# Performance work log

Measured on AMD Instinct MI355X. Metric: run time of the kernel, lower is better.

Reference implementation:

```python
import jax, jax.numpy as jnp
import numpy as np

ROPE_THETA = 10000.0

def _apply_rope(x, theta=ROPE_THETA):
    # x: [B, H, L, d_head]
    L, d_k = x.shape[-2], x.shape[-1]
    inv_freq = 1.0 / (theta ** (jnp.arange(0, d_k, 2, dtype=jnp.float32) / d_k))  # [d_k/2]
    ang = jnp.arange(L, dtype=jnp.float32)[:, None] * inv_freq[None, :]           # [L, d_k/2]
    ang = jnp.repeat(ang, 2, axis=-1)                                             # [L, d_k] interleaved
    xr = x.reshape(x.shape[:-1] + (d_k // 2, 2))
    rot = jnp.stack((-xr[..., 1], xr[..., 0]), axis=-1).reshape(x.shape)
    return x * jnp.cos(ang) + rot * jnp.sin(ang)

def setup_inputs() -> dict:
    key = jax.random.key(0)
    k1, k2, k3 = jax.random.split(key, 3)
    B, L, D = 2, 2048, 2048
    std_qkv = np.sqrt(2.0 / (D + 3 * D)).astype(np.float32)
    std_o = np.sqrt(2.0 / (D + D)).astype(np.float32)
    return {
        "x": jax.random.normal(k1, (B, L, D), dtype=jnp.float32),
        "W_qkv": jax.random.normal(k2, (3 * D, D), dtype=jnp.float32) * std_qkv,
        "W_o": jax.random.normal(k3, (D, D), dtype=jnp.float32) * std_o,
    }

def reference(x, W_qkv, W_o):
    B, L, D = x.shape
    H = 16
    dh = D // H
    qkv = jnp.einsum('bld,ed->ble', x, W_qkv)            # [B, L, 3D]
    q, k, v = jnp.split(qkv, 3, axis=-1)
    # [B, H, L, dh]
    q = q.reshape(B, L, H, dh).transpose(0, 2, 1, 3)
    k = k.reshape(B, L, H, dh).transpose(0, 2, 1, 3)
    v = v.reshape(B, L, H, dh).transpose(0, 2, 1, 3)
    q = _apply_rope(q)
    k = _apply_rope(k)
    scale = 1.0 / np.sqrt(dh).astype(np.float32)
    att = jnp.einsum('bhqd,bhkd->bhqk', q, k) * scale    # [B, H, L, L]
    causal = jnp.tril(jnp.ones((L, L), dtype=bool))
    att = jnp.where(causal, att, -jnp.inf)
    p = jax.nn.softmax(att, axis=-1)
    y = jnp.einsum('bhqk,bhkd->bhqd', p, v)              # [B, H, L, dh]
    y = y.transpose(0, 2, 1, 3).reshape(B, L, D)
    return jnp.einsum('bld,ed->ble', y, W_o)
```

## Files before the change

kernel.cpp:

```cpp
#include <hip/hip_runtime.h>
#include <math.h>

typedef __bf16 bf16x8 __attribute__((ext_vector_type(8)));
typedef float f32x4 __attribute__((ext_vector_type(4)));
typedef unsigned short us8 __attribute__((ext_vector_type(8)));

#define B_ 2
#define L_ 2048
#define D_ 2048
#define H_ 16
#define DH 128

__device__ __forceinline__ unsigned short f2b(float f) {
  union { float f; unsigned u; } v; v.f = f;
  unsigned u = v.u;
  return (unsigned short)((u + 0x7fffu + ((u >> 16) & 1u)) >> 16);
}
__device__ __forceinline__ float b2f(unsigned short h) {
  union { unsigned u; float f; } v; v.u = ((unsigned)h) << 16;
  return v.f;
}

#define GLD16(g, l) __builtin_amdgcn_global_load_lds(                          \
    (const __attribute__((address_space(1))) void*)(g),                        \
    (__attribute__((address_space(3))) void*)(l), 16, 0, 0)

#define SBAR() __builtin_amdgcn_s_barrier()
#define LGK0() asm volatile("s_waitcnt lgkmcnt(0)")
#define SCB0() __builtin_amdgcn_sched_barrier(0)
#define VMC3() asm volatile("s_waitcnt vmcnt(3)" ::: "memory")
#define VMC0() asm volatile("s_waitcnt vmcnt(0)" ::: "memory")

__device__ __forceinline__ unsigned ldsoff(const void* p) {
  return (unsigned)(unsigned long long)(const __attribute__((address_space(3))) char*)p;
}
__device__ __forceinline__ bf16x8 dsr128(unsigned a) {
  bf16x8 r;
  asm volatile("ds_read_b128 %0, %1" : "=v"(r) : "v"(a));
  return r;
}

__global__ void f32_to_bf16_3(const float* __restrict__ a, int na4,
                              const float* __restrict__ b, int nb4,
                              const float* __restrict__ c, int nc4,
                              unsigned short* __restrict__ oa,
                              unsigned short* __restrict__ ob,
                              unsigned short* __restrict__ oc) {
  const int total = na4 + nb4 + nc4;
  int i = blockIdx.x * blockDim.x + threadIdx.x;
  const int stride = gridDim.x * blockDim.x;
  for (; i < total; i += stride) {
    const float* src;
    unsigned short* dst;
    int j = i;
    if (j < na4) { src = a; dst = oa; }
    else if (j < na4 + nb4) { j -= na4; src = b; dst = ob; }
    else { j -= na4 + nb4; src = c; dst = oc; }
    const float4 v = ((const float4*)src)[j];
    ushort4 o;
    o.x = f2b(v.x); o.y = f2b(v.y); o.z = f2b(v.z); o.w = f2b(v.w);
    ((ushort4*)dst)[j] = o;
  }
}

template <bool OUT_BF16>
__global__ __launch_bounds__(512, 4)
void gemmk32(const unsigned short* __restrict__ A,
             const unsigned short* __restrict__ Bm,
             void* __restrict__ Cv, int M, int N, int K) {
  __shared__ __align__(16) unsigned short lA[3][128 * 32];
  __shared__ __align__(16) unsigned short lB[3][256 * 32];
  const int tid = threadIdx.x;
  const int w = tid >> 6, lane = tid & 63;
  const int lo = lane & 15, hi = lane >> 4;
  const int mh = w >> 2;
  const int wn = (w & 3) * 64;
  const int GM = M >> 7;
  const int nwg = gridDim.x;
  const int f = blockIdx.x;
  const int v = (f & 7) * (nwg >> 3) + (f >> 3);
  const int bn = v / GM, bm = v % GM;
  const int NT = K >> 5;

  const int srow = tid >> 2;
  const int gs = (tid & 3) ^ ((srow >> 1) & 3);
  auto stA = [&](int buf, int tile) {
    GLD16(A + (long)(bm * 128 + srow) * K + tile * 32 + gs * 8,
          &lA[buf][(tid & ~63) * 8]);
  };
  auto stB = [&](int buf, int u, int tile) {
    GLD16(Bm + (long)(bn * 256 + u * 128 + srow) * K + tile * 32 + gs * 8,
          &lB[buf][u * 4096 + (tid & ~63) * 8]);
  };

  unsigned aoff[4], boff[4];
#pragma unroll
  for (int mi = 0; mi < 4; ++mi) {
    const int r = mh * 64 + mi * 16 + lo;
    aoff[mi] = ldsoff(&lA[0][0]) + r * 64 + ((hi ^ ((r >> 1) & 3)) * 16);
  }
#pragma unroll
  for (int ni = 0; ni < 4; ++ni) {
    const int rb = wn + ni * 16 + lo;
    boff[ni] = ldsoff(&lB[0][0]) + rb * 64 + ((hi ^ ((rb >> 1) & 3)) * 16);
  }

  f32x4 acc[4][4] = {};

  stA(0, 0); stB(0, 0, 0); stB(0, 1, 0);
  stA(1, 1); stB(1, 0, 1); stB(1, 1, 1);
  VMC3();
  SBAR();

  for (int t = 0; t < NT; ++t) {
    const int bt = t % 3;
    const int b2 = (t + 2) % 3;
    const bool nx = (t + 2 < NT);
    const unsigned ab = (unsigned)(bt * 8192);
    const unsigned bb = (unsigned)(bt * 16384);
    bf16x8 af[4], bfv[4];
#pragma unroll
    for (int mi = 0; mi < 4; ++mi) af[mi] = dsr128(aoff[mi] + ab);
#pragma unroll
    for (int ni = 0; ni < 4; ++ni) bfv[ni] = dsr128(boff[ni] + bb);
    if (nx) { stA(b2, t + 2); stB(b2, 0, t + 2); stB(b2, 1, t + 2); }
    LGK0(); SCB0();
    __builtin_amdgcn_s_setprio(1);
#pragma unroll
    for (int mi = 0; mi < 4; ++mi)
#pragma unroll
      for (int ni = 0; ni < 4; ++ni)
        acc[mi][ni] = __builtin_amdgcn_mfma_f32_16x16x32_bf16(
            af[mi], bfv[ni], acc[mi][ni], 0, 0, 0);
    __builtin_amdgcn_s_setprio(0);
    if (t < NT - 2) VMC3(); else VMC0();
    SBAR();
  }

  const int r0 = bm * 128 + mh * 64;
  const int c0 = bn * 256 + wn;
#pragma unroll
  for (int mi = 0; mi < 4; ++mi) {
#pragma unroll
    for (int r = 0; r < 4; ++r) {
      const long row = r0 + mi * 16 + hi * 4 + r;
#pragma unroll
      for (int ni = 0; ni < 4; ++ni) {
        const int col = c0 + ni * 16 + lo;
        if (OUT_BF16)
          ((unsigned short*)Cv)[row * N + col] = f2b(acc[mi][ni][r]);
        else
          ((float*)Cv)[row * N + col] = acc[mi][ni][r];
      }
    }
  }
}

__global__ void rope_qk(const unsigned short* __restrict__ qkv,
                        unsigned short* __restrict__ Qo,
                        unsigned short* __restrict__ Ko) {
  const int idx = blockIdx.x * 256 + threadIdx.x;
  const int i = idx & 63;
  const int l = (idx >> 6) & (L_ - 1);
  const int h = (idx >> 17) & (H_ - 1);
  const int b = idx >> 21;
  const float invf = exp2f(-(float)i * 0.20762050593045077f);
  const float ang = (float)l * invf;
  float sn, cs;
  sincosf(ang, &sn, &cs);
  const long base = ((long)b * L_ + l) * (3 * D_) + h * DH + 2 * i;
  const unsigned qin = *(const unsigned*)&qkv[base];
  const unsigned kin = *(const unsigned*)&qkv[base + D_];
  const float q0 = b2f((unsigned short)qin), q1 = b2f((unsigned short)(qin >> 16));
  const float k0 = b2f((unsigned short)kin), k1 = b2f((unsigned short)(kin >> 16));
  const float sc = 0.12751743f;
  const float qo0 = (q0 * cs - q1 * sn) * sc, qo1 = (q1 * cs + q0 * sn) * sc;
  const float ko0 = (k0 * cs - k1 * sn), ko1 = (k1 * cs + k0 * sn);
  const long oo = ((long)(b * H_ + h) * L_ + l) * DH + 2 * i;
  *(unsigned*)&Qo[oo] = (unsigned)f2b(qo0) | ((unsigned)f2b(qo1) << 16);
  *(unsigned*)&Ko[oo] = (unsigned)f2b(ko0) | ((unsigned)f2b(ko1) << 16);
}

__global__ __launch_bounds__(256)
void v_fragpack(const unsigned short* __restrict__ qkv,
                unsigned short* __restrict__ Vf) {
  const int lblk = blockIdx.x;
  const int bh = blockIdx.y;
  const int b = bh >> 4, h = bh & 15;
  __shared__ unsigned short tile[64 * 137];
  const int tid = threadIdx.x;
  const int l0 = lblk * 64;
#pragma unroll
  for (int j = 0; j < 4; ++j) {
    const int c = j * 256 + tid;
    const int row = c >> 4, col8 = c & 15;
    const us8 v = *(const us8*)&qkv[((long)b * L_ + l0 + row) * (3 * D_) +
                                    2 * D_ + h * DH + col8 * 8];
    unsigned short* dst = &tile[row * 137 + col8 * 8];
#pragma unroll
    for (int e = 0; e < 8; ++e) dst[e] = v[e];
  }
  __syncthreads();
#pragma unroll
  for (int j = 0; j < 4; ++j) {
    const int c = j * 256 + tid;
    const int k32l = c >> 9, t2 = (c >> 6) & 7, lane = c & 63;
    const int lo = lane & 15, hi = lane >> 4;
    us8 v;
#pragma unroll
    for (int e = 0; e < 8; ++e)
      v[e] = tile[(k32l * 32 + hi * 8 + e) * 137 + t2 * 16 + lo];
    *(us8*)&Vf[(((size_t)bh * 64 + lblk * 2 + k32l) * 8 + t2) * 512 + lane * 8] = v;
  }
}

__global__ __launch_bounds__(256, 2)
void flash_attn3(const unsigned short* __restrict__ Q,
                 const unsigned short* __restrict__ Kg,
                 const unsigned short* __restrict__ Vf,
                 unsigned short* __restrict__ Y) {
  const int p = blockIdx.x;
  const int tA = p, tB = (L_ / 64 - 1) - p;
  const int h = blockIdx.y, b = blockIdx.z;
  const int tid = threadIdx.x;
  const int wave = tid >> 6, lane = tid & 63;
  const int lo = lane & 15, hi = lane >> 4;
  const int swz = (lo & 7) << 4;
  const int qA = tA * 64 + wave * 16;
  const int qB = tB * 64 + wave * 16;
  const long hoff = ((long)(b * H_ + h)) * L_ * DH;
  const unsigned short* Qh = Q + hoff;
  const unsigned short* Kh = Kg + hoff;
  const unsigned short* Vfh = Vf + ((size_t)(b * H_ + h)) * (64 * 8 * 512);

  __shared__ unsigned short lK[2][64 * 128];
  __shared__ unsigned short pl[4][2][16 * 72];
  unsigned short* plA = &pl[wave][0][0];
  unsigned short* plB = &pl[wave][1][0];

  auto stage = [&](int bufi, int kv0s) {
    unsigned short* bk = &lK[bufi][0];
#pragma unroll
    for (int j = 0; j < 4; ++j) {
      const int c = j * 256 + tid;
      const int row = c >> 4;
      const int soff = ((c & 15) ^ (row & 7)) << 3;
      GLD16(Kh + (long)(kv0s + row) * DH + soff, &bk[(c & ~63) * 8]);
    }
  };

  bf16x8 qfA[4], qfB[4];
#pragma unroll
  for (int s = 0; s < 4; ++s) {
    qfA[s] = *(const bf16x8*)&Qh[(long)(qA + lo) * DH + s * 32 + hi * 8];
    qfB[s] = *(const bf16x8*)&Qh[(long)(qB + lo) * DH + s * 32 + hi * 8];
  }

  float mA = -INFINITY, lsA = 0.f, mB = -INFINITY, lsB = 0.f;
  f32x4 yA[8] = {}, yB[8] = {};

  auto softmax = [&](f32x4 (&st)[4], float& m, float& lsum, f32x4 (&yacc)[8],
                     unsigned short* plw, int qw, int kv0) {
    if (kv0 + 63 > qw) {
      const int d0 = qw + lo - kv0 - hi * 4;
#pragma unroll
      for (int t = 0; t < 4; ++t) {
        const int dt = d0 - t * 16;
#pragma unroll
        for (int r = 0; r < 4; ++r)
          if (r > dt) st[t][r] = -INFINITY;
      }
    }
    float tm0 = fmaxf(fmaxf(st[0][0], st[0][1]), fmaxf(st[0][2], st[0][3]));
    float tm1 = fmaxf(fmaxf(st[1][0], st[1][1]), fmaxf(st[1][2], st[1][3]));
    float tm2 = fmaxf(fmaxf(st[2][0], st[2][1]), fmaxf(st[2][2], st[2][3]));
    float tm3 = fmaxf(fmaxf(st[3][0], st[3][1]), fmaxf(st[3][2], st[3][3]));
    float rm = fmaxf(fmaxf(tm0, tm1), fmaxf(tm2, tm3));
    rm = fmaxf(rm, __shfl_xor(rm, 16));
    rm = fmaxf(rm, __shfl_xor(rm, 32));
    if (!__all(rm <= m + 8.f)) {
      const float mn = fmaxf(m, rm);
      const float alpha = exp2f(m - mn);
      m = mn;
      lsum *= alpha;
      float ar[4];
#pragma unroll
      for (int r = 0; r < 4; ++r) ar[r] = __shfl(alpha, hi * 4 + r);
#pragma unroll
      for (int t2 = 0; t2 < 8; ++t2)
#pragma unroll
        for (int r = 0; r < 4; ++r) yacc[t2][r] *= ar[r];
    }
    float rs = 0.f;
#pragma unroll
    for (int t = 0; t < 4; ++t) {
#pragma unroll
      for (int r2 = 0; r2 < 2; ++r2) {
        const float e0 = exp2f(st[t][2 * r2] - m);
        const float e1 = exp2f(st[t][2 * r2 + 1] - m);
        rs += e0 + e1;
        const unsigned short u0 = __builtin_bit_cast(unsigned short, (__bf16)e0);
        const unsigned short u1 = __builtin_bit_cast(unsigned short, (__bf16)e1);
        *(unsigned*)&plw[lo * 72 + t * 16 + hi * 4 + 2 * r2] =
            (unsigned)u0 | ((unsigned)u1 << 16);
      }
    }
    rs += __shfl_xor(rs, 16);
    rs += __shfl_xor(rs, 32);
    lsum += rs;
  };

  const int nIter = tB + 1;
  stage(0, 0);
  __syncthreads();

  for (int it = 0; it < nIter; ++it) {
    const int kv0 = it * 64;
    const bool aAct = (it <= tA);
    if (it + 1 < nIter) stage((it + 1) & 1, kv0 + 64);
    const char* bkc = (const char*)&lK[it & 1][0];
    f32x4 stA[4] = {}, stB[4] = {};
    if (aAct) {
#pragma unroll
      for (int s = 0; s < 4; ++s) {
        const int inner = (lo * 256 + s * 64 + hi * 16) ^ swz;
#pragma unroll
        for (int t = 0; t < 4; ++t) {
          const bf16x8 kf = *(const bf16x8*)(bkc + t * 4096 + inner);
          stA[t] = __builtin_amdgcn_mfma_f32_16x16x32_bf16(kf, qfA[s], stA[t], 0, 0, 0);
          stB[t] = __builtin_amdgcn_mfma_f32_16x16x32_bf16(kf, qfB[s], stB[t], 0, 0, 0);
        }
      }
    } else {
#pragma unroll
      for (int s = 0; s < 4; ++s) {
        const int inner = (lo * 256 + s * 64 + hi * 16) ^ swz;
#pragma unroll
        for (int t = 0; t < 4; ++t) {
          const bf16x8 kf = *(const bf16x8*)(bkc + t * 4096 + inner);
          stB[t] = __builtin_amdgcn_mfma_f32_16x16x32_bf16(kf, qfB[s], stB[t], 0, 0, 0);
        }
      }
    }
    if (aAct) softmax(stA, mA, lsA, yA, plA, qA, kv0);
    softmax(stB, mB, lsB, yB, plB, qB, kv0);
    const unsigned short* vbase = Vfh + (size_t)(it * 16) * 512 + lane * 8;
#pragma unroll
    for (int kt = 0; kt < 2; ++kt) {
      bf16x8 vf[8];
#pragma unroll
      for (int t2 = 0; t2 < 8; ++t2)
        vf[t2] = *(const bf16x8*)(vbase + (size_t)(kt * 8 + t2) * 512);
      const bf16x8 pfB = *(const bf16x8*)&plB[lo * 72 + kt * 32 + hi * 8];
#pragma unroll
      for (int t2 = 0; t2 < 8; ++t2)
        yB[t2] = __builtin_amdgcn_mfma_f32_16x16x32_bf16(pfB, vf[t2], yB[t2], 0, 0, 0);
      if (aAct) {
        const bf16x8 pfA = *(const bf16x8*)&plA[lo * 72 + kt * 32 + hi * 8];
#pragma unroll
        for (int t2 = 0; t2 < 8; ++t2)
          yA[t2] = __builtin_amdgcn_mfma_f32_16x16x32_bf16(pfA, vf[t2], yA[t2], 0, 0, 0);
      }
    }
    __syncthreads();
  }

  auto wout = [&](f32x4 (&yacc)[8], float lsum, int qw) {
    const float inv = 1.f / lsum;
    float ir[4];
#pragma unroll
    for (int r = 0; r < 4; ++r) ir[r] = __shfl(inv, hi * 4 + r);
#pragma unroll
    for (int r = 0; r < 4; ++r) {
      const long row = qw + hi * 4 + r;
      unsigned short* yrow = Y + ((long)b * L_ + row) * D_ + h * DH;
#pragma unroll
      for (int t2 = 0; t2 < 8; ++t2)
        yrow[t2 * 16 + lo] = f2b(yacc[t2][r] * ir[r]);
    }
  };
  wout(yA, lsA, qA);
  wout(yB, lsB, qB);
}

extern "C" void kernel_launch(void* const* d_in, const int* in_sizes, int n_in,
                              void* d_out, int out_size, void* d_ws, size_t ws_size,
                              hipStream_t stream) {
  const float* x = (const float*)d_in[0];
  const float* wqkv = (const float*)d_in[1];
  const float* wo = (const float*)d_in[2];
  float* out = (float*)d_out;

  unsigned short* ws = (unsigned short*)d_ws;
  const size_t N_X = (size_t)B_ * L_ * D_;
  const size_t N_WQKV = (size_t)3 * D_ * D_;
  const size_t N_WO = (size_t)D_ * D_;
  const size_t N_QKV = (size_t)B_ * L_ * 3 * D_;
  const size_t N_HEAD = (size_t)B_ * H_ * L_ * DH;
  unsigned short* xb = ws;
  unsigned short* wqkb = xb + N_X;
  unsigned short* wob = wqkb + N_WQKV;
  unsigned short* qkv = wob + N_WO;
  unsigned short* Qb = qkv + N_QKV;
  unsigned short* Kb = Qb + N_HEAD;
  unsigned short* Vf = Kb + N_HEAD;
  unsigned short* Yb = Vf + N_HEAD;
  const size_t need = (size_t)(Yb + N_HEAD - ws) * sizeof(unsigned short);
  if (ws_size < need) return;

  f32_to_bf16_3<<<2048, 256, 0, stream>>>(
      x, (int)(N_X / 4), wqkv, (int)(N_WQKV / 4), wo, (int)(N_WO / 4),
      xb, wqkb, wob);

  gemmk32<true><<<(B_ * L_ / 128) * (3 * D_ / 256), 512, 0, stream>>>(
      xb, wqkb, qkv, B_ * L_, 3 * D_, D_);

  rope_qk<<<(B_ * H_ * L_ * 64) / 256, 256, 0, stream>>>(qkv, Qb, Kb);
  v_fragpack<<<dim3(L_ / 64, B_ * H_), 256, 0, stream>>>(qkv, Vf);

  flash_attn3<<<dim3(16, H_, B_), 256, 0, stream>>>(Qb, Kb, Vf, Yb);

  gemmk32<false><<<(B_ * L_ / 128) * (D_ / 256), 512, 0, stream>>>(
      Yb, wob, out, B_ * L_, D_, D_);
}
```

Baseline: 286.0 us.

## Add 256x256 ping-pong GEMM for QKV projection and prefetch V fragments early

Introduces a new GEMM kernel with 256x256 output tiles, K=64 double-buffered LDS stages split into halves, XOR-swizzled LDS layout, and interleaved MFMA clusters with setprio and staged vmcnt waits. It replaces the 128x256 K=32 GEMM for the QKV projection, aiming for higher arithmetic intensity and better overlap of global loads with MFMA work. Separately, in attention, all 16 V fragments are loaded before softmax so their global latency hides behind softmax math. This raises register pressure (acc[8][4] plus fragments, vf[16]) and reduces the grid size, which risks occupancy or tail effects.

Result: no change. 286.1 us (+0.0%).

```diff
diff --git a/kernel.cpp b/kernel.cpp
--- a/kernel.cpp
+++ b/kernel.cpp
@@ -27,9 +27,11 @@
 
 #define SBAR() __builtin_amdgcn_s_barrier()
 #define LGK0() asm volatile("s_waitcnt lgkmcnt(0)")
-#define SCB0() __builtin_amdgcn_sched_barrier(0)
+#define VMC8() asm volatile("s_waitcnt vmcnt(8)" ::: "memory")
+#define VMC4() asm volatile("s_waitcnt vmcnt(4)" ::: "memory")
 #define VMC3() asm volatile("s_waitcnt vmcnt(3)" ::: "memory")
 #define VMC0() asm volatile("s_waitcnt vmcnt(0)" ::: "memory")
+#define SCB0() __builtin_amdgcn_sched_barrier(0)
 
 __device__ __forceinline__ unsigned ldsoff(const void* p) {
   return (unsigned)(unsigned long long)(const __attribute__((address_space(3))) char*)p;
@@ -60,6 +62,125 @@
     ushort4 o;
     o.x = f2b(v.x); o.y = f2b(v.y); o.z = f2b(v.z); o.w = f2b(v.w);
     ((ushort4*)dst)[j] = o;
+  }
+}
+
+#define LOAD_A8(BUF, MH)                                                       \
+  _Pragma("unroll") for (int q = 0; q < 4; ++q) {                              \
+    const int rh = (MH) * 64 + q * 16 + lo;                                    \
+    _Pragma("unroll") for (int s = 0; s < 2; ++s)                              \
+        af[q][s] = *(const bf16x8*)&lA[BUF][wm]                                \
+            [rh * 64 + (((s * 4 + hi) ^ (rh & 7)) * 8)];                       \
+  }
+
+#define LOAD_B8(BUF, NH)                                                       \
+  _Pragma("unroll") for (int j = 0; j < 2; ++j) {                              \
+    const int rb = blb + (NH) * 32 + j * 16 + lo;                              \
+    _Pragma("unroll") for (int s = 0; s < 2; ++s)                              \
+        bfr[NH][j][s] = *(const bf16x8*)&lB[BUF][hb]                           \
+            [rb * 64 + (((s * 4 + hi) ^ (rb & 7)) * 8)];                       \
+  }
+
+#define MFMA16P(MH, NH)                                                        \
+  do {                                                                         \
+    __builtin_amdgcn_s_setprio(1);                                             \
+    _Pragma("unroll") for (int q = 0; q < 4; ++q)                              \
+        _Pragma("unroll") for (int j = 0; j < 2; ++j)                          \
+            _Pragma("unroll") for (int s = 0; s < 2; ++s)                      \
+                acc[(MH) * 4 + q][(NH) * 2 + j] =                              \
+                    __builtin_amdgcn_mfma_f32_16x16x32_bf16(                   \
+                        af[q][s], bfr[NH][j][s],                               \
+                        acc[(MH) * 4 + q][(NH) * 2 + j], 0, 0, 0);             \
+    __builtin_amdgcn_s_setprio(0);                                             \
+  } while (0)
+
+template <bool OUT_BF16>
+__global__ __launch_bounds__(512)
+void gemm8x(const unsigned short* __restrict__ A,
+            const unsigned short* __restrict__ Bm,
+            void* __restrict__ Cv, int M, int N, int K) {
+  __shared__ __align__(16) unsigned short lA[2][2][128 * 64];
+  __shared__ __align__(16) unsigned short lB[2][2][128 * 64];
+  const int tid = threadIdx.x;
+  const int w = tid >> 6, lane = tid & 63;
+  const int lo = lane & 15, hi = lane >> 4;
+  const int wm = w >> 2;
+  const int wn4 = w & 3;
+  const int hb = wn4 >> 1;
+  const int blb = (wn4 & 1) * 64;
+  const int GM = M >> 8;
+  const int f = blockIdx.x;
+  const int v = (f & 7) * (gridDim.x >> 3) + (f >> 3);
+  const int bn = v / GM, bm = v % GM;
+  const int NI = K >> 7;
+
+  const int row64 = tid >> 3;
+  const int gs = (tid & 7) ^ (row64 & 7);
+  auto stA = [&](int buf, int h, int tile) {
+#pragma unroll
+    for (int u = 0; u < 2; ++u)
+      GLD16(A + (long)(bm * 256 + h * 128 + u * 64 + row64) * K + tile * 64 + gs * 8,
+            &lA[buf][h][u * 4096 + (tid & ~63) * 8]);
+  };
+  auto stB = [&](int buf, int h, int tile) {
+#pragma unroll
+    for (int u = 0; u < 2; ++u)
+      GLD16(Bm + (long)(bn * 256 + h * 128 + u * 64 + row64) * K + tile * 64 + gs * 8,
+            &lB[buf][h][u * 4096 + (tid & ~63) * 8]);
+  };
+
+  f32x4 acc[8][4] = {};
+  bf16x8 af[4][2], bfr[2][2][2];
+
+  stB(0, 0, 0); stB(0, 1, 0); stA(0, 0, 0); stA(0, 1, 0);
+  stB(1, 0, 1); stB(1, 1, 1); stA(1, 0, 1); stA(1, 1, 1);
+  VMC8();
+  SBAR();
+
+  for (int i = 0; i < NI; ++i) {
+    const int t2n = 2 * i + 2;
+    const bool nx = (i + 1 < NI);
+    LOAD_A8(0, 0) LOAD_B8(0, 0)
+    SBAR(); LGK0(); MFMA16P(0, 0); SBAR();
+    LOAD_B8(0, 1)
+    SBAR(); LGK0(); MFMA16P(0, 1); SBAR();
+    LOAD_A8(0, 1)
+    if (nx) stB(0, 0, t2n);
+    SBAR(); LGK0(); MFMA16P(1, 1); SBAR();
+    if (nx) stB(0, 1, t2n);
+    SBAR(); MFMA16P(1, 0);
+    if (nx) VMC4(); else VMC0();
+    SBAR();
+    LOAD_A8(1, 0) LOAD_B8(1, 0)
+    if (nx) { stA(0, 0, t2n); stA(0, 1, t2n); }
+    SBAR(); LGK0(); MFMA16P(0, 0); SBAR();
+    LOAD_B8(1, 1)
+    SBAR(); LGK0(); MFMA16P(0, 1); SBAR();
+    LOAD_A8(1, 1)
+    if (nx) { stB(1, 0, t2n + 1); stB(1, 1, t2n + 1); }
+    SBAR(); LGK0(); MFMA16P(1, 1); SBAR();
+    if (nx) { stA(1, 0, t2n + 1); stA(1, 1, t2n + 1); }
+    SBAR(); MFMA16P(1, 0);
+    if (nx) VMC8();
+    SBAR();
+  }
+
+  const int r0 = bm * 256 + wm * 128;
+  const int c0 = bn * 256 + wn4 * 64;
+#pragma unroll
+  for (int mi = 0; mi < 8; ++mi) {
+#pragma unroll
+    for (int r = 0; r < 4; ++r) {
+      const long row = r0 + mi * 16 + hi * 4 + r;
+#pragma unroll
+      for (int ni = 0; ni < 4; ++ni) {
+        const int col = c0 + ni * 16 + lo;
+        if (OUT_BF16)
+          ((unsigned short*)Cv)[row * N + col] = f2b(acc[mi][ni][r]);
+        else
+          ((float*)Cv)[row * N + col] = acc[mi][ni][r];
+      }
+    }
   }
 }
 
@@ -342,24 +463,24 @@
         }
       }
     }
+    const unsigned short* vbase = Vfh + (size_t)(it * 16) * 512 + lane * 8;
+    bf16x8 vf[16];
+#pragma unroll
+    for (int t2 = 0; t2 < 16; ++t2)
+      vf[t2] = *(const bf16x8*)(vbase + (size_t)t2 * 512);
     if (aAct) softmax(stA, mA, lsA, yA, plA, qA, kv0);
     softmax(stB, mB, lsB, yB, plB, qB, kv0);
-    const unsigned short* vbase = Vfh + (size_t)(it * 16) * 512 + lane * 8;
 #pragma unroll
     for (int kt = 0; kt < 2; ++kt) {
-      bf16x8 vf[8];
+      const bf16x8 pfB = *(const bf16x8*)&plB[lo * 72 + kt * 32 + hi * 8];
 #pragma unroll
       for (int t2 = 0; t2 < 8; ++t2)
-        vf[t2] = *(const bf16x8*)(vbase + (size_t)(kt * 8 + t2) * 512);
-      const bf16x8 pfB = *(const bf16x8*)&plB[lo * 72 + kt * 32 + hi * 8];
-#pragma unroll
-      for (int t2 = 0; t2 < 8; ++t2)
-        yB[t2] = __builtin_amdgcn_mfma_f32_16x16x32_bf16(pfB, vf[t2], yB[t2], 0, 0, 0);
+        yB[t2] = __builtin_amdgcn_mfma_f32_16x16x32_bf16(pfB, vf[kt * 8 + t2], yB[t2], 0, 0, 0);
       if (aAct) {
         const bf16x8 pfA = *(const bf16x8*)&plA[lo * 72 + kt * 32 + hi * 8];
 #pragma unroll
         for (int t2 = 0; t2 < 8; ++t2)
-          yA[t2] = __builtin_amdgcn_mfma_f32_16x16x32_bf16(pfA, vf[t2], yA[t2], 0, 0, 0);
+          yA[t2] = __builtin_amdgcn_mfma_f32_16x16x32_bf16(pfA, vf[kt * 8 + t2], yA[t2], 0, 0, 0);
       }
     }
     __syncthreads();
@@ -412,7 +533,7 @@
       x, (int)(N_X / 4), wqkv, (int)(N_WQKV / 4), wo, (int)(N_WO / 4),
       xb, wqkb, wob);
 
-  gemmk32<true><<<(B_ * L_ / 128) * (3 * D_ / 256), 512, 0, stream>>>(
+  gemm8x<true><<<(B_ * L_ / 256) * (3 * D_ / 256), 512, 0, stream>>>(
       xb, wqkb, qkv, B_ * L_, 3 * D_, D_);
 
   rope_qk<<<(B_ * H_ * L_ * 64) / 256, 256, 0, stream>>>(qkv, Qb, Kb);
```

## Add 4-wave 64x128-per-wave GEMM for QKV projection and prefetch V earlier

Applied to the files above, without the earlier changes.

Adds a new GEMM kernel that uses 256 threads, with each wave computing a 64x128 output tile (4x8 MFMA fragments) over a triple-buffered LDS pipeline. The QKV projection now uses it instead of the 8-wave kernel. The goal is more register-level reuse of A and B fragments per LDS read, at the cost of higher register pressure and lower occupancy. In flash attention, all 16 V fragments are now loaded before the softmax, so global load latency overlaps the softmax math, which costs more VGPRs.

After: 278.0 us. -2.8%, faster.

```diff
diff --git a/kernel.cpp b/kernel.cpp
--- a/kernel.cpp
+++ b/kernel.cpp
@@ -28,6 +28,7 @@
 #define SBAR() __builtin_amdgcn_s_barrier()
 #define LGK0() asm volatile("s_waitcnt lgkmcnt(0)")
 #define SCB0() __builtin_amdgcn_sched_barrier(0)
+#define VMC6() asm volatile("s_waitcnt vmcnt(6)" ::: "memory")
 #define VMC3() asm volatile("s_waitcnt vmcnt(3)" ::: "memory")
 #define VMC0() asm volatile("s_waitcnt vmcnt(0)" ::: "memory")
 
@@ -60,6 +61,105 @@
     ushort4 o;
     o.x = f2b(v.x); o.y = f2b(v.y); o.z = f2b(v.z); o.w = f2b(v.w);
     ((ushort4*)dst)[j] = o;
+  }
+}
+
+template <bool OUT_BF16>
+__global__ __launch_bounds__(256, 2)
+void gemmw128(const unsigned short* __restrict__ A,
+              const unsigned short* __restrict__ Bm,
+              void* __restrict__ Cv, int M, int N, int K) {
+  __shared__ __align__(16) unsigned short lA[3][128 * 32];
+  __shared__ __align__(16) unsigned short lB[3][256 * 32];
+  const int tid = threadIdx.x;
+  const int w = tid >> 6, lane = tid & 63;
+  const int lo = lane & 15, hi = lane >> 4;
+  const int mh = w >> 1;
+  const int nh = w & 1;
+  const int GM = M >> 7;
+  const int nwg = gridDim.x;
+  const int f = blockIdx.x;
+  const int v = (f & 7) * (nwg >> 3) + (f >> 3);
+  const int bn = v / GM, bm = v % GM;
+  const int NT = K >> 5;
+
+  const int srow = tid >> 2;
+  const int gs = (tid & 3) ^ ((srow >> 1) & 3);
+  auto stA = [&](int buf, int u, int tile) {
+    GLD16(A + (long)(bm * 128 + u * 64 + srow) * K + tile * 32 + gs * 8,
+          &lA[buf][u * 2048 + tid * 8]);
+  };
+  auto stB = [&](int buf, int u, int tile) {
+    GLD16(Bm + (long)(bn * 256 + u * 64 + srow) * K + tile * 32 + gs * 8,
+          &lB[buf][u * 2048 + tid * 8]);
+  };
+
+  unsigned aoff[4], boff[8];
+#pragma unroll
+  for (int mi = 0; mi < 4; ++mi) {
+    const int r = mh * 64 + mi * 16 + lo;
+    aoff[mi] = ldsoff(&lA[0][0]) + r * 64 + ((hi ^ ((r >> 1) & 3)) * 16);
+  }
+#pragma unroll
+  for (int ni = 0; ni < 8; ++ni) {
+    const int rb = nh * 128 + ni * 16 + lo;
+    boff[ni] = ldsoff(&lB[0][0]) + rb * 64 + ((hi ^ ((rb >> 1) & 3)) * 16);
+  }
+
+  f32x4 acc[4][8] = {};
+
+  stA(0, 0, 0); stA(0, 1, 0);
+  stB(0, 0, 0); stB(0, 1, 0); stB(0, 2, 0); stB(0, 3, 0);
+  stA(1, 0, 1); stA(1, 1, 1);
+  stB(1, 0, 1); stB(1, 1, 1); stB(1, 2, 1); stB(1, 3, 1);
+  VMC6();
+  SBAR();
+
+  for (int t = 0; t < NT; ++t) {
+    const int bt = t % 3;
+    const int b2 = (t + 2) % 3;
+    const bool nx = (t + 2 < NT);
+    const unsigned ab = (unsigned)(bt * 8192);
+    const unsigned bb = (unsigned)(bt * 16384);
+    bf16x8 af[4], bfv[8];
+#pragma unroll
+    for (int mi = 0; mi < 4; ++mi) af[mi] = dsr128(aoff[mi] + ab);
+#pragma unroll
+    for (int ni = 0; ni < 8; ++ni) bfv[ni] = dsr128(boff[ni] + bb);
+    if (nx) {
+      stA(b2, 0, t + 2); stA(b2, 1, t + 2);
+      stB(b2, 0, t + 2); stB(b2, 1, t + 2);
+      stB(b2, 2, t + 2); stB(b2, 3, t + 2);
+    }
+    LGK0(); SCB0();
+    __builtin_amdgcn_s_setprio(1);
+#pragma unroll
+    for (int ni = 0; ni < 8; ++ni)
+#pragma unroll
+      for (int mi = 0; mi < 4; ++mi)
+        acc[mi][ni] = __builtin_amdgcn_mfma_f32_16x16x32_bf16(
+            af[mi], bfv[ni], acc[mi][ni], 0, 0, 0);
+    __builtin_amdgcn_s_setprio(0);
+    if (t < NT - 2) VMC6(); else VMC0();
+    SBAR();
+  }
+
+  const int r0 = bm * 128 + mh * 64;
+  const int c0 = bn * 256 + nh * 128;
+#pragma unroll
+  for (int mi = 0; mi < 4; ++mi) {
+#pragma unroll
+    for (int r = 0; r < 4; ++r) {
+      const long row = r0 + mi * 16 + hi * 4 + r;
+#pragma unroll
+      for (int ni = 0; ni < 8; ++ni) {
+        const int col = c0 + ni * 16 + lo;
+        if (OUT_BF16)
+          ((unsigned short*)Cv)[row * N + col] = f2b(acc[mi][ni][r]);
+        else
+          ((float*)Cv)[row * N + col] = acc[mi][ni][r];
+      }
+    }
   }
 }
 
@@ -342,24 +442,24 @@
         }
       }
     }
+    const unsigned short* vbase = Vfh + (size_t)(it * 16) * 512 + lane * 8;
+    bf16x8 vf[16];
+#pragma unroll
+    for (int t2 = 0; t2 < 16; ++t2)
+      vf[t2] = *(const bf16x8*)(vbase + (size_t)t2 * 512);
     if (aAct) softmax(stA, mA, lsA, yA, plA, qA, kv0);
     softmax(stB, mB, lsB, yB, plB, qB, kv0);
-    const unsigned short* vbase = Vfh + (size_t)(it * 16) * 512 + lane * 8;
 #pragma unroll
     for (int kt = 0; kt < 2; ++kt) {
-      bf16x8 vf[8];
+      const bf16x8 pfB = *(const bf16x8*)&plB[lo * 72 + kt * 32 + hi * 8];
 #pragma unroll
       for (int t2 = 0; t2 < 8; ++t2)
-        vf[t2] = *(const bf16x8*)(vbase + (size_t)(kt * 8 + t2) * 512);
-      const bf16x8 pfB = *(const bf16x8*)&plB[lo * 72 + kt * 32 + hi * 8];
-#pragma unroll
-      for (int t2 = 0; t2 < 8; ++t2)
-        yB[t2] = __builtin_amdgcn_mfma_f32_16x16x32_bf16(pfB, vf[t2], yB[t2], 0, 0, 0);
+        yB[t2] = __builtin_amdgcn_mfma_f32_16x16x32_bf16(pfB, vf[kt * 8 + t2], yB[t2], 0, 0, 0);
       if (aAct) {
         const bf16x8 pfA = *(const bf16x8*)&plA[lo * 72 + kt * 32 + hi * 8];
 #pragma unroll
         for (int t2 = 0; t2 < 8; ++t2)
-          yA[t2] = __builtin_amdgcn_mfma_f32_16x16x32_bf16(pfA, vf[t2], yA[t2], 0, 0, 0);
+          yA[t2] = __builtin_amdgcn_mfma_f32_16x16x32_bf16(pfA, vf[kt * 8 + t2], yA[t2], 0, 0, 0);
       }
     }
     __syncthreads();
@@ -412,7 +512,7 @@
       x, (int)(N_X / 4), wqkv, (int)(N_WQKV / 4), wo, (int)(N_WO / 4),
       xb, wqkb, wob);
 
-  gemmk32<true><<<(B_ * L_ / 128) * (3 * D_ / 256), 512, 0, stream>>>(
+  gemmw128<true><<<(B_ * L_ / 128) * (3 * D_ / 256), 256, 0, stream>>>(
       xb, wqkb, qkv, B_ * L_, 3 * D_, D_);
 
   rope_qk<<<(B_ * H_ * L_ * 64) / 256, 256, 0, stream>>>(qkv, Qb, Kb);
```
